# Optimization experiments

Measured on AMD Instinct MI355X. Metric: run time of the kernel, lower is better.

The kernel has to match this reference:

```python
import jax, jax.numpy as jnp
import numpy as np

# Network dimensions (match init_kwargs)
N_IN, N_HID, N_OUT = 2048, 8192, 1024
N = N_IN + N_HID + N_OUT
BATCH = 512


def setup_inputs() -> dict:
    key = jax.random.key(0)
    k_w, k_b, k_x = jax.random.split(key, 3)
    # GraphNet._init_connections: Xavier-ish std based on (n_inputs + n_outputs)
    std = (2.0 / (N_IN + N_OUT)) ** 0.5
    W = jax.random.normal(k_w, (N, N), dtype=jnp.float32) * std
    # mask: inputs -> hidden, hidden -> outputs (fixed 3-level DAG)
    mask = jnp.zeros((N, N), dtype=jnp.float32)
    mask = mask.at[:N_IN, N_IN:N_IN + N_HID].set(1.0)
    mask = mask.at[N_IN:N_IN + N_HID, N_IN + N_HID:].set(1.0)
    # bias is zero-init in the module; use small random values so it is exercised
    bias = jax.random.normal(k_b, (N,), dtype=jnp.float32) * 0.01
    x = jax.random.normal(k_x, (BATCH, N_IN), dtype=jnp.float32)
    return {"x": x, "W": W, "bias": bias, "mask": mask}


def reference(x, W, bias, mask):
    # Faithful translation of GraphNet.forward for the canonical 3-level
    # topology produced by _init_connections/_compute_levels:
    #   level 0: input nodes [0, N_IN)
    #   level 1: hidden nodes [N_IN, N_IN+N_HID)  -> ReLU
    #   level 2: output nodes [N_IN+N_HID, N)     -> identity (OUTPUT type)
    W_eff = W * mask                       # [N, N] masked adjacency
    B = x.shape[0]
    h = jnp.zeros((B, N), dtype=x.dtype).at[:, :N_IN].set(x)
    # level 1 (hidden): pre_act = h @ W_eff[:, idx] + bias[idx]; ReLU
    pre_h = h @ W_eff[:, N_IN:N_IN + N_HID] + bias[N_IN:N_IN + N_HID]
    h = h.at[:, N_IN:N_IN + N_HID].set(jax.nn.relu(pre_h))
    # level 2 (outputs): pre-activation only (node_type == OUTPUT -> no ReLU)
    pre_o = h @ W_eff[:, N_IN + N_HID:] + bias[N_IN + N_HID:]
    return pre_o                            # h[:, output_indices]
```

## Files before the change

### kernel.cpp

```cpp
#include <hip/hip_runtime.h>

#define N_IN 2048
#define N_HID 8192
#define N_OUT 1024
#define NTOT 11264

typedef __attribute__((ext_vector_type(4))) float f32x4;
typedef __attribute__((ext_vector_type(4))) short short4v;
typedef __attribute__((ext_vector_type(8))) short short8v;
typedef __attribute__((ext_vector_type(2))) unsigned u32x2;

__device__ inline short f2bf(float f) {
    unsigned u = __float_as_uint(f);
    return (short)((u + 0x7fffu + ((u >> 16) & 1u)) >> 16);
}

__device__ inline unsigned cvt_pk_bf16(float lo, float hi) {
    unsigned r;
    asm("v_cvt_pk_bf16_f32 %0, %1, %2" : "=v"(r) : "v"(lo), "v"(hi));
    return r;
}

__device__ inline int perm64(int c) {
    return (c & 32) + (((c >> 2) & 3) << 3) + (((c >> 4) & 1) << 2) + (c & 3);
}

__device__ inline void gload_lds16(const void* g, void* l) {
    __builtin_amdgcn_global_load_lds(
        (const __attribute__((address_space(1))) unsigned int*)g,
        (__attribute__((address_space(3))) unsigned int*)l, 16, 0, 0);
}

__global__ __launch_bounds__(256) void cvt_x(
    const float* __restrict__ x, short* __restrict__ xb)
{
    const int i = blockIdx.x * 256 + threadIdx.x;
    const f32x4 v = *reinterpret_cast<const f32x4*>(x + (size_t)i * 4);
    u32x2 s;
    s[0] = cvt_pk_bf16(v[0], v[1]);
    s[1] = cvt_pk_bf16(v[2], v[3]);
    const int c0  = (i * 4) & (N_IN - 1);
    const int p   = (c0 & ~63) + perm64(c0 & 63);
    const size_t row = (size_t)(i >> 9);
    *reinterpret_cast<u32x2*>(xb + row * N_IN + p) = s;
}

template<bool FUSE>
__global__ __launch_bounds__(512, 4) void gemm_bf16(
    const short* __restrict__ A,
    const float* __restrict__ W,
    const float* __restrict__ bias,
    short* __restrict__ hOut,
    float* __restrict__ pOut,
    int lda, int nt, int wrow0, int wcol0)
{
    __shared__ __align__(16) short As[3][128 * 64];
    __shared__ __align__(16) short Bs[2][128 * 64];

    const int t    = threadIdx.x;
    const int lane = t & 63;
    const int wid  = t >> 6;
    const int wr   = wid >> 2;
    const int wc   = wid & 3;
    const int brow = blockIdx.y * 128;
    const int bcol = blockIdx.x * 128;
    const int l15  = lane & 15;
    const int lg   = lane >> 4;
    const int ks   = blockIdx.z * 1024;

    const int arow = lane >> 3;
    const int asw  = ((lane & 7) * 16) ^ (arow << 4);

    const int nb   = (lane & 7) + 8 * (wid >> 1);
    const int kblk = ((lane >> 3) & 7) + 8 * (wid & 1);
    const int n0 = nb * 4, k0 = kblk * 4;
    const int p0 = perm64(k0);

    const char*  Abytes = (const char*)A;
    const size_t lda_b  = (size_t)lda * 2;

    const char* aG0 = Abytes + (size_t)(brow + (wid * 2 + 0) * 8 + arow) * lda_b
                             + (size_t)ks * 2 + asw;
    const char* aG1 = Abytes + (size_t)(brow + (wid * 2 + 1) * 8 + arow) * lda_b
                             + (size_t)ks * 2 + asw;
    const int ldsAoff = wid * 2048;

    f32x4 acc[4][2] = {};
    f32x4 bvE[4], bvO[4];

    const float* wp0 = &W[(size_t)(wrow0 + ks + k0) * NTOT + (wcol0 + bcol + n0)];

#define B_LOAD(TT, BV) { \
    const float* wp = wp0 + (size_t)(TT) * 64 * NTOT; \
    _Pragma("unroll") for (int j = 0; j < 4; ++j) \
        BV[j] = *reinterpret_cast<const f32x4*>(wp + (size_t)j * NTOT); }

#define A_LOAD(TT, DST) { \
    gload_lds16(aG0 + (size_t)(TT) * 128, (char*)(DST) + ldsAoff); \
    gload_lds16(aG1 + (size_t)(TT) * 128, (char*)(DST) + ldsAoff + 1024); }

#define B_WRITE(TT, BV) { \
    char* bsb = (char*)Bs + ((TT) & 1) * 16384; \
    _Pragma("unroll") for (int i = 0; i < 4; ++i) { \
        u32x2 s; \
        s[0] = cvt_pk_bf16(BV[0][i], BV[1][i]); \
        s[1] = cvt_pk_bf16(BV[2][i], BV[3][i]); \
        const int r = n0 + i; \
        *reinterpret_cast<u32x2*>( \
            bsb + (((r * 128) + p0 * 2) ^ ((r & 7) << 4))) = s; } }

#define COMPUTE(TT, AB) { \
    const char* bb = (const char*)Bs + ((TT) & 1) * 16384; \
    _Pragma("unroll") for (int g = 0; g < 2; ++g) { \
        const int koff = g * 64 + lg * 16; \
        short8v a[4], b[2]; \
        _Pragma("unroll") for (int m = 0; m < 4; ++m) { \
            const int r = wr * 64 + m * 16 + l15; \
            a[m] = *reinterpret_cast<const short8v*>( \
                (const char*)(AB) + ((r * 128 + koff) ^ ((r & 7) << 4))); } \
        _Pragma("unroll") for (int n = 0; n < 2; ++n) { \
            const int r = wc * 32 + n * 16 + l15; \
            b[n] = *reinterpret_cast<const short8v*>( \
                bb + ((r * 128 + koff) ^ ((r & 7) << 4))); } \
        __builtin_amdgcn_s_setprio(1); \
        _Pragma("unroll") for (int m = 0; m < 4; ++m) \
          _Pragma("unroll") for (int n = 0; n < 2; ++n) \
            acc[m][n] = __builtin_amdgcn_mfma_f32_16x16x32_bf16( \
                a[m], b[n], acc[m][n], 0, 0, 0); \
        __builtin_amdgcn_s_setprio(0); } }

#define WAITV(N) { asm volatile("s_waitcnt vmcnt(" #N ")" ::: "memory"); \
                   __builtin_amdgcn_sched_barrier(0); }
#define BARRIER  { asm volatile("s_waitcnt lgkmcnt(0)" ::: "memory"); \
                   __builtin_amdgcn_sched_barrier(0); \
                   __builtin_amdgcn_s_barrier(); \
                   __builtin_amdgcn_sched_barrier(0); }
#define ROTATE   { char* rtmp = (char*)aR; aR = aM; aM = aW; aW = rtmp; }

    const char* aR = (const char*)As;
    const char* aM = (const char*)As + 16384;
    char*       aW = (char*)As + 32768;

    B_LOAD(0, bvE); A_LOAD(0, As);
    B_LOAD(1, bvO); A_LOAD(1, (char*)As + 16384);
    WAITV(6);
    B_WRITE(0, bvE);
    BARRIER;

    for (int tt = 0; tt + 2 < nt; tt += 2) {
        B_LOAD(tt + 2, bvE); A_LOAD(tt + 2, aW);
        WAITV(6);
        B_WRITE(tt + 1, bvO);
        COMPUTE(tt, aR);
        BARRIER;
        ROTATE;
        B_LOAD(tt + 3, bvO); A_LOAD(tt + 3, aW);
        WAITV(6);
        B_WRITE(tt + 2, bvE);
        COMPUTE(tt + 1, aR);
        BARRIER;
        ROTATE;
    }

    WAITV(0);
    B_WRITE(nt - 1, bvO);
    COMPUTE(nt - 2, aR);
    BARRIER;
    COMPUTE(nt - 1, aM);

#undef B_LOAD
#undef A_LOAD
#undef B_WRITE
#undef COMPUTE
#undef WAITV
#undef BARRIER
#undef ROTATE

    if (FUSE) {
#pragma unroll
        for (int m = 0; m < 4; ++m) {
            const int row0 = brow + wr * 64 + m * 16 + lg * 4;
#pragma unroll
            for (int n = 0; n < 2; ++n) {
                const int col  = bcol + wc * 32 + n * 16 + l15;
                const int pcol = (col & ~63) + perm64(col & 63);
                const float bb = bias[N_IN + col];
#pragma unroll
                for (int q = 0; q < 4; ++q) {
                    float v = acc[m][n][q] + bb;
                    v = v > 0.f ? v : 0.f;
                    hOut[(size_t)(row0 + q) * N_HID + pcol] = f2bf(v);
                }
            }
        }
    } else {
        float* po = pOut + (size_t)blockIdx.z * (512 * N_OUT);
#pragma unroll
        for (int m = 0; m < 4; ++m) {
            const int row0 = brow + wr * 64 + m * 16 + lg * 4;
#pragma unroll
            for (int n = 0; n < 2; ++n) {
                const int col = bcol + wc * 32 + n * 16 + l15;
#pragma unroll
                for (int q = 0; q < 4; ++q)
                    po[(size_t)(row0 + q) * N_OUT + col] = acc[m][n][q];
            }
        }
    }
}

__global__ __launch_bounds__(256) void reduce_bias(
    const float* __restrict__ part,
    const float* __restrict__ bias,
    float* __restrict__ out)
{
    const int idx = (blockIdx.x * 256 + threadIdx.x) * 4;
    f32x4 s = *reinterpret_cast<const f32x4*>(&bias[N_IN + N_HID + (idx & 1023)]);
#pragma unroll
    for (int sp = 0; sp < 8; ++sp)
        s += *reinterpret_cast<const f32x4*>(&part[(size_t)sp * 524288 + idx]);
    *reinterpret_cast<f32x4*>(&out[idx]) = s;
}

extern "C" void kernel_launch(void* const* d_in, const int* in_sizes, int n_in,
                              void* d_out, int out_size, void* d_ws, size_t ws_size,
                              hipStream_t stream) {
    const float* x    = (const float*)d_in[0];
    const float* W    = (const float*)d_in[1];
    const float* bias = (const float*)d_in[2];
    float* out = (float*)d_out;

    short* h    = (short*)d_ws;
    float* part = (float*)((char*)d_ws + (size_t)(8 << 20));
    short* xb   = (short*)((char*)d_ws + (size_t)(8 << 20));

    cvt_x<<<dim3(1024), dim3(256), 0, stream>>>(x, xb);

    gemm_bf16<true><<<dim3(64, 4, 1), dim3(512), 0, stream>>>(
        xb, W, bias, h, nullptr, N_IN, 32, 0, N_IN);

    gemm_bf16<false><<<dim3(8, 4, 8), dim3(512), 0, stream>>>(
        h, W, nullptr, nullptr, part, N_HID, 16, N_IN, N_IN + N_HID);

    reduce_bias<<<dim3(512), dim3(256), 0, stream>>>(part, bias, out);
}
```

Baseline: 72.03 us.

## Split each K-tile into two barrier-synchronized phases interleaving loads with MFMA

Restructures the GEMM main loop into a ping-pong style schedule. Each 64-wide K tile now runs as two half-phases, and each half-phase issues half of the next tile's global and LDS loads, crosses a workgroup barrier, and then runs eight MFMAs at raised priority. The aim is to interleave memory issue with matrix work across the waves and to spread the load traffic more evenly through the loop. In exchange it adds two extra s_barriers per phase, which adds synchronization overhead and may serialize the waves more.

Measured after the change: 159.9 us. +121.9%, slower.

```diff
diff --git a/kernel.cpp b/kernel.cpp
--- a/kernel.cpp
+++ b/kernel.cpp
@@ -90,14 +90,13 @@
 
     const float* wp0 = &W[(size_t)(wrow0 + ks + k0) * NTOT + (wcol0 + bcol + n0)];
 
-#define B_LOAD(TT, BV) { \
-    const float* wp = wp0 + (size_t)(TT) * 64 * NTOT; \
-    _Pragma("unroll") for (int j = 0; j < 4; ++j) \
-        BV[j] = *reinterpret_cast<const f32x4*>(wp + (size_t)j * NTOT); }
-
-#define A_LOAD(TT, DST) { \
-    gload_lds16(aG0 + (size_t)(TT) * 128, (char*)(DST) + ldsAoff); \
-    gload_lds16(aG1 + (size_t)(TT) * 128, (char*)(DST) + ldsAoff + 1024); }
+#define B_LOAD_H(TT, BV, H) { \
+    const float* wp = wp0 + (size_t)(TT) * 64 * NTOT + (size_t)(2 * (H)) * NTOT; \
+    BV[2 * (H)]     = *reinterpret_cast<const f32x4*>(wp); \
+    BV[2 * (H) + 1] = *reinterpret_cast<const f32x4*>(wp + NTOT); }
+
+#define A_LOAD_H0(TT) gload_lds16(aG0 + (size_t)(TT) * 128, aW + ldsAoff);
+#define A_LOAD_H1(TT) gload_lds16(aG1 + (size_t)(TT) * 128, aW + ldsAoff + 1024);
 
 #define B_WRITE(TT, BV) { \
     char* bsb = (char*)Bs + ((TT) & 1) * 16384; \
@@ -109,72 +108,85 @@
         *reinterpret_cast<u32x2*>( \
             bsb + (((r * 128) + p0 * 2) ^ ((r & 7) << 4))) = s; } }
 
-#define COMPUTE(TT, AB) { \
-    const char* bb = (const char*)Bs + ((TT) & 1) * 16384; \
-    _Pragma("unroll") for (int g = 0; g < 2; ++g) { \
-        const int koff = g * 64 + lg * 16; \
-        short8v a[4], b[2]; \
-        _Pragma("unroll") for (int m = 0; m < 4; ++m) { \
-            const int r = wr * 64 + m * 16 + l15; \
-            a[m] = *reinterpret_cast<const short8v*>( \
-                (const char*)(AB) + ((r * 128 + koff) ^ ((r & 7) << 4))); } \
-        _Pragma("unroll") for (int n = 0; n < 2; ++n) { \
-            const int r = wc * 32 + n * 16 + l15; \
-            b[n] = *reinterpret_cast<const short8v*>( \
-                bb + ((r * 128 + koff) ^ ((r & 7) << 4))); } \
-        __builtin_amdgcn_s_setprio(1); \
-        _Pragma("unroll") for (int m = 0; m < 4; ++m) \
-          _Pragma("unroll") for (int n = 0; n < 2; ++n) \
-            acc[m][n] = __builtin_amdgcn_mfma_f32_16x16x32_bf16( \
-                a[m], b[n], acc[m][n], 0, 0, 0); \
-        __builtin_amdgcn_s_setprio(0); } }
-
 #define WAITV(N) { asm volatile("s_waitcnt vmcnt(" #N ")" ::: "memory"); \
                    __builtin_amdgcn_sched_barrier(0); }
 #define BARRIER  { asm volatile("s_waitcnt lgkmcnt(0)" ::: "memory"); \
                    __builtin_amdgcn_sched_barrier(0); \
                    __builtin_amdgcn_s_barrier(); \
                    __builtin_amdgcn_sched_barrier(0); }
-#define ROTATE   { char* rtmp = (char*)aR; aR = aM; aM = aW; aW = rtmp; }
-
-    const char* aR = (const char*)As;
-    const char* aM = (const char*)As + 16384;
-    char*       aW = (char*)As + 32768;
-
-    B_LOAD(0, bvE); A_LOAD(0, As);
-    B_LOAD(1, bvO); A_LOAD(1, (char*)As + 16384);
+#define ROTATE   { char* rtmp = aR; aR = aM; aM = aW; aW = rtmp; }
+
+#define PHASE(TT, G, STAGE, SYNC) { \
+    const char* ab = aR; \
+    const char* bb = (const char*)Bs + ((TT) & 1) * 16384; \
+    const int koff = (G) * 64 + lg * 16; \
+    const int ax   = (l15 & 7) << 4; \
+    short8v a0, a1, a2, a3, b0, b1; \
+    { const int r0 = wr * 64 + l15; \
+      a0 = *reinterpret_cast<const short8v*>(ab + (((r0     ) * 128 + koff) ^ ax)); \
+      a1 = *reinterpret_cast<const short8v*>(ab + (((r0 + 16) * 128 + koff) ^ ax)); \
+      a2 = *reinterpret_cast<const short8v*>(ab + (((r0 + 32) * 128 + koff) ^ ax)); \
+      a3 = *reinterpret_cast<const short8v*>(ab + (((r0 + 48) * 128 + koff) ^ ax)); \
+      const int rb = wc * 32 + l15; \
+      b0 = *reinterpret_cast<const short8v*>(bb + (((rb     ) * 128 + koff) ^ ax)); \
+      b1 = *reinterpret_cast<const short8v*>(bb + (((rb + 16) * 128 + koff) ^ ax)); } \
+    STAGE; \
+    SYNC; \
+    __builtin_amdgcn_s_barrier(); \
+    asm volatile("s_waitcnt lgkmcnt(0)" ::: "memory"); \
+    __builtin_amdgcn_sched_barrier(0); \
+    __builtin_amdgcn_s_setprio(1); \
+    acc[0][0] = __builtin_amdgcn_mfma_f32_16x16x32_bf16(a0, b0, acc[0][0], 0, 0, 0); \
+    acc[0][1] = __builtin_amdgcn_mfma_f32_16x16x32_bf16(a0, b1, acc[0][1], 0, 0, 0); \
+    acc[1][0] = __builtin_amdgcn_mfma_f32_16x16x32_bf16(a1, b0, acc[1][0], 0, 0, 0); \
+    acc[1][1] = __builtin_amdgcn_mfma_f32_16x16x32_bf16(a1, b1, acc[1][1], 0, 0, 0); \
+    acc[2][0] = __builtin_amdgcn_mfma_f32_16x16x32_bf16(a2, b0, acc[2][0], 0, 0, 0); \
+    acc[2][1] = __builtin_amdgcn_mfma_f32_16x16x32_bf16(a2, b1, acc[2][1], 0, 0, 0); \
+    acc[3][0] = __builtin_amdgcn_mfma_f32_16x16x32_bf16(a3, b0, acc[3][0], 0, 0, 0); \
+    acc[3][1] = __builtin_amdgcn_mfma_f32_16x16x32_bf16(a3, b1, acc[3][1], 0, 0, 0); \
+    __builtin_amdgcn_s_setprio(0); \
+    __builtin_amdgcn_s_barrier(); \
+    __builtin_amdgcn_sched_barrier(0); }
+
+    char* aR = (char*)As;
+    char* aM = (char*)As + 16384;
+    char* aW = (char*)As + 32768;
+
+    B_LOAD_H(0, bvE, 0); B_LOAD_H(0, bvE, 1);
+    gload_lds16(aG0, aR + ldsAoff);
+    gload_lds16(aG1, aR + ldsAoff + 1024);
+    B_LOAD_H(1, bvO, 0); B_LOAD_H(1, bvO, 1);
+    gload_lds16(aG0 + 128, aM + ldsAoff);
+    gload_lds16(aG1 + 128, aM + ldsAoff + 1024);
     WAITV(6);
     B_WRITE(0, bvE);
     BARRIER;
 
     for (int tt = 0; tt + 2 < nt; tt += 2) {
-        B_LOAD(tt + 2, bvE); A_LOAD(tt + 2, aW);
-        WAITV(6);
-        B_WRITE(tt + 1, bvO);
-        COMPUTE(tt, aR);
-        BARRIER;
+        PHASE(tt, 0, { A_LOAD_H0(tt + 2); B_LOAD_H(tt + 2, bvE, 0); }, (void)0);
+        PHASE(tt, 1, { A_LOAD_H1(tt + 2); B_LOAD_H(tt + 2, bvE, 1); },
+                     { WAITV(6); B_WRITE(tt + 1, bvO); });
         ROTATE;
-        B_LOAD(tt + 3, bvO); A_LOAD(tt + 3, aW);
-        WAITV(6);
-        B_WRITE(tt + 2, bvE);
-        COMPUTE(tt + 1, aR);
-        BARRIER;
+        PHASE(tt + 1, 0, { A_LOAD_H0(tt + 3); B_LOAD_H(tt + 3, bvO, 0); }, (void)0);
+        PHASE(tt + 1, 1, { A_LOAD_H1(tt + 3); B_LOAD_H(tt + 3, bvO, 1); },
+                         { WAITV(6); B_WRITE(tt + 2, bvE); });
         ROTATE;
     }
 
-    WAITV(0);
-    B_WRITE(nt - 1, bvO);
-    COMPUTE(nt - 2, aR);
-    BARRIER;
-    COMPUTE(nt - 1, aM);
-
-#undef B_LOAD
-#undef A_LOAD
+    PHASE(nt - 2, 0, (void)0, (void)0);
+    PHASE(nt - 2, 1, (void)0, { WAITV(0); B_WRITE(nt - 1, bvO); });
+    ROTATE;
+    PHASE(nt - 1, 0, (void)0, (void)0);
+    PHASE(nt - 1, 1, (void)0, (void)0);
+
+#undef B_LOAD_H
+#undef A_LOAD_H0
+#undef A_LOAD_H1
 #undef B_WRITE
-#undef COMPUTE
 #undef WAITV
 #undef BARRIER
 #undef ROTATE
+#undef PHASE
 
     if (FUSE) {
 #pragma unroll
```
